# Kernel tuning notes

Measured on AMD Instinct MI355X. Metric: run time of the kernel, lower is better.

The kernel has to match this reference:

```python
import jax, jax.numpy as jnp
import numpy as np


def setup_inputs() -> dict:
    key = jax.random.key(0)
    ks = jax.random.split(key, 16)
    B, S, D = 2, 2048, 1024
    H, SH, RH = 16, 1, 3
    hd = D // H
    w = 1.0 / np.sqrt(D)
    return {
        "x": jax.random.normal(ks[0], (B, S, D), jnp.float32),
        "Wq": jax.random.normal(ks[1], (D, D), jnp.float32) * w,
        "bq": jnp.zeros((D,), jnp.float32),
        "Wk": jax.random.normal(ks[2], (D, D), jnp.float32) * w,
        "bk": jnp.zeros((D,), jnp.float32),
        "Wv": jax.random.normal(ks[3], (D, D), jnp.float32) * w,
        "bv": jnp.zeros((D,), jnp.float32),
        "Wproj": jax.random.normal(ks[4], (D, D), jnp.float32) * w,
        "bproj": jnp.zeros((D,), jnp.float32),
        "Wr": jax.random.normal(ks[5], (D, H - SH), jnp.float32) * w,
        "br": jnp.zeros((H - SH,), jnp.float32),
        "Ws": jax.random.normal(ks[6], (D, 2), jnp.float32) * w,
        "bs": jnp.zeros((2,), jnp.float32),
        "temperature": jnp.zeros((H, 1, 1), jnp.float32),
        "query_embedding": jax.random.truncated_normal(ks[7], -2.0, 2.0, (H, 1, hd), jnp.float32) * 0.02,
        "num_heads": H,
        "shared_heads": SH,
        "routed_heads": RH,
    }


def reference(x, Wq, bq, Wk, bk, Wv, bv, Wproj, bproj, Wr, br, Ws, bs,
              temperature, query_embedding, num_heads, shared_heads, routed_heads):
    B, S, D = x.shape
    H = num_heads
    hd = D // H

    def split_heads(t):  # [B,S,D] -> [B,H,S,hd]
        return t.reshape(B, S, H, hd).transpose(0, 2, 1, 3)

    q = split_heads(x @ Wq + bq)
    k = split_heads(x @ Wk + bk)
    v = split_heads(x @ Wv + bv)

    # L2-normalize q along head_dim, add learned query embedding, scale by softplus(temperature)
    q_norm = q * jax.lax.rsqrt(jnp.sum(q * q, axis=-1, keepdims=True) + 1e-12)
    q_scaled = (q_norm + query_embedding[None]) * jax.nn.softplus(temperature)[None]

    attn = jnp.einsum('bhqd,bhkd->bhqk', q_scaled, k) / jnp.sqrt(jnp.float32(hd))
    attn = jax.nn.softmax(attn, axis=-1)
    o = jnp.einsum('bhqk,bhkd->bhqd', attn, v)
    o = o.transpose(0, 2, 1, 3).reshape(B, S, D)  # [B,S,D]

    # Routed-head gating via top-k router
    gates = jax.nn.softmax(o @ Wr + br, axis=-1)          # [B,S,H-SH]
    _, idx = jax.lax.top_k(gates, routed_heads)           # [B,S,RH]
    mask = jax.nn.one_hot(idx, H - shared_heads, dtype=gates.dtype).sum(axis=2)
    routed_gates = gates * mask * jnp.float32(routed_heads)

    # Shared-head gating
    sw = jax.nn.softmax(o @ Ws + bs, axis=-1)             # [B,S,2]
    shared_gates = sw * jnp.float32(shared_heads)
    w0 = sw * 2.0
    shared_gates = w0[..., 0:1] * shared_gates
    routed_gates = w0[..., 1:2] * routed_gates
    masked_gates = jnp.concatenate([shared_gates, routed_gates], axis=-1)

    # einsum('bnh,bnd->bnd') sums over h: scales o by sum of gates
    o = masked_gates.sum(axis=-1, keepdims=True) * o
    return o @ Wproj + bproj
```

## Files before the change

### kernel.cpp

```cpp
#include <hip/hip_runtime.h>
#include <hip/hip_bf16.h>

typedef unsigned short ushort_t;
typedef unsigned int uint_t;

typedef __attribute__((ext_vector_type(8))) short bf8;
typedef __attribute__((ext_vector_type(4))) float f4;
typedef __attribute__((ext_vector_type(16))) float f16v;

__device__ __forceinline__ float bf2f(ushort_t u) {
    unsigned int x = ((unsigned int)u) << 16;
    return __uint_as_float(x);
}
__device__ __forceinline__ ushort_t f2bf(float f) {
    unsigned int x = __float_as_uint(f);
    unsigned int r = x + 0x7fffu + ((x >> 16) & 1u);
    return (ushort_t)(r >> 16);
}
__device__ __forceinline__ uint_t pack2bf(float a, float b) {
    return (uint_t)f2bf(a) | ((uint_t)f2bf(b) << 16);
}
__device__ __forceinline__ uint_t pack2bf_fast(float a, float b) {
    uint_t au = __float_as_uint(a) + 0x8000u;
    uint_t bu = __float_as_uint(b) + 0x8000u;
    return __builtin_amdgcn_perm(bu, au, 0x07060302);
}
__device__ __forceinline__ float exp2_fast(float x) {
    float r; asm("v_exp_f32 %0, %1" : "=v"(r) : "v"(x)); return r;
}
__device__ __forceinline__ uint_t cvtpk_bf16(float lo, float hi) {
    uint_t r; asm("v_cvt_pk_bf16_f32 %0, %1, %2" : "=v"(r) : "v"(lo), "v"(hi)); return r;
}
__device__ __forceinline__ void pl32swap(uint_t &a, uint_t &b) {
    asm("v_permlane32_swap_b32 %0, %1" : "+v"(a), "+v"(b));
}

__device__ __forceinline__ void gl2lds16(const ushort_t* g, ushort_t* l) {
    __builtin_amdgcn_global_load_lds(
        (const __attribute__((address_space(1))) void*)g,
        (__attribute__((address_space(3))) void*)l, 16, 0, 0);
}

__device__ __forceinline__ void waitl0() {
    asm volatile("s_waitcnt lgkmcnt(0)" ::: "memory");
    __builtin_amdgcn_sched_barrier(0);
}

__global__ __launch_bounds__(256)
void prep(const float* __restrict__ x, ushort_t* __restrict__ xb,
          const float* __restrict__ Wr, const float* __restrict__ Ws,
          ushort_t* __restrict__ Wg,
          const float* __restrict__ W0, const float* __restrict__ W1,
          const float* __restrict__ W2, const float* __restrict__ W3,
          ushort_t* __restrict__ T0, ushort_t* __restrict__ T1,
          ushort_t* __restrict__ T2, ushort_t* __restrict__ T3)
{
    __shared__ float tile[32][33];
    int bid = blockIdx.x;
    int t = threadIdx.x;
    if (bid < 4096) {
        int i = bid * 256 + t;
        float4 v = ((const float4*)x)[i];
        uint2 o;
        o.x = pack2bf(v.x, v.y);
        o.y = pack2bf(v.z, v.w);
        ((uint2*)xb)[i] = o;
    } else if (bid < 4224) {
        int idx = (bid - 4096) * 256 + t;
        int c = idx >> 10, d = idx & 1023;
        float v = 0.f;
        if (c < 15) v = Wr[(size_t)d * 15 + c];
        else if (c < 17) v = Ws[(size_t)d * 2 + (c - 15)];
        Wg[idx] = f2bf(v);
    } else {
        int idx = bid - 4224;
        int z = idx >> 10, r10 = idx & 1023;
        int k0 = (r10 & 31) * 32, n0 = (r10 >> 5) * 32;
        const float* W; ushort_t* T;
        switch (z) {
            case 0: W = W0; T = T0; break;
            case 1: W = W1; T = T1; break;
            case 2: W = W2; T = T2; break;
            default: W = W3; T = T3; break;
        }
        int r = t >> 3, c4 = (t & 7) * 4;
        float4 v = *(const float4*)&W[(size_t)(k0 + r) * 1024 + n0 + c4];
        tile[r][c4 + 0] = v.x; tile[r][c4 + 1] = v.y;
        tile[r][c4 + 2] = v.z; tile[r][c4 + 3] = v.w;
        __syncthreads();
        int n = t >> 3, kk = (t & 7) * 4;
        uint2 o;
        o.x = pack2bf(tile[kk][n], tile[kk + 1][n]);
        o.y = pack2bf(tile[kk + 2][n], tile[kk + 3][n]);
        *(uint2*)&T[(size_t)(n0 + n) * 1024 + k0 + kk] = o;
    }
}

__global__ __launch_bounds__(256)
void gemmQKV(const ushort_t* __restrict__ A, const ushort_t* __restrict__ Wt3,
             const float* __restrict__ bq, const float* __restrict__ bk,
             const float* __restrict__ bv,
             ushort_t* __restrict__ Qb, ushort_t* __restrict__ Kw,
             ushort_t* __restrict__ VTw,
             const float* __restrict__ temp, const float* __restrict__ emb)
{
    const int K = 1024;
    __shared__ ushort_t As[128 * 64];
    __shared__ ushort_t Bs[64 * 64];

    int t = threadIdx.x;
    int m0 = blockIdx.x * 128;
    int y = blockIdx.y;
    int region = y >> 4;
    int n0r = (y & 15) * 64;
    int head = y & 15;

    int lane = t & 63, w = t >> 6;
    int lm = lane & 15, quad = lane >> 4;
    int wm = w * 32;

    f4 acc[8] = {};

    int srow = t >> 3;
    int schunk = ((t & 7) ^ (srow & 7)) * 8;
    const ushort_t* pA = &A[(size_t)(m0 + srow) * K + schunk];
    const ushort_t* pB = &Wt3[(size_t)(y * 64 + srow) * K + schunk];
    const size_t rstep = (size_t)32 * K;

    for (int k0 = 0; k0 < K; k0 += 64) {
        #pragma unroll
        for (int j = 0; j < 4; j++)
            gl2lds16(pA + j * rstep, &As[(t + j * 256) * 8]);
        #pragma unroll
        for (int j = 0; j < 2; j++)
            gl2lds16(pB + j * rstep, &Bs[(t + j * 256) * 8]);
        pA += 64; pB += 64;
        __syncthreads();

        #pragma unroll
        for (int ks = 0; ks < 2; ks++) {
            int rc = ((ks * 4 + quad) ^ (lm & 7)) * 8;
            bf8 af[2], bfr[4];
            #pragma unroll
            for (int mi = 0; mi < 2; mi++)
                af[mi] = *(bf8*)&As[(wm + mi * 16 + lm) * 64 + rc];
            #pragma unroll
            for (int ni = 0; ni < 4; ni++)
                bfr[ni] = *(bf8*)&Bs[(ni * 16 + lm) * 64 + rc];
            if (region == 2) {
                #pragma unroll
                for (int mi = 0; mi < 2; mi++)
                #pragma unroll
                for (int ni = 0; ni < 4; ni++)
                    acc[mi * 4 + ni] = __builtin_amdgcn_mfma_f32_16x16x32_bf16(af[mi], bfr[ni], acc[mi * 4 + ni], 0, 0, 0);
            } else {
                #pragma unroll
                for (int ni = 0; ni < 4; ni++)
                #pragma unroll
                for (int mi = 0; mi < 2; mi++)
                    acc[ni * 2 + mi] = __builtin_amdgcn_mfma_f32_16x16x32_bf16(bfr[ni], af[mi], acc[ni * 2 + mi], 0, 0, 0);
            }
        }
        __syncthreads();
    }

    if (region == 0) {
        float sp = log1pf(__expf(temp[head]));
        float qs = sp * 0.18033688011112042f;
        f4 bv4[4], ev4[4];
        #pragma unroll
        for (int ni = 0; ni < 4; ni++) {
            bv4[ni] = *(const f4*)&bq[n0r + ni * 16 + quad * 4];
            ev4[ni] = *(const f4*)&emb[head * 64 + ni * 16 + quad * 4];
        }
        #pragma unroll
        for (int mi = 0; mi < 2; mi++) {
            float v[4][4];
            float ss = 0.f;
            #pragma unroll
            for (int ni = 0; ni < 4; ni++)
            #pragma unroll
            for (int i = 0; i < 4; i++) {
                v[ni][i] = acc[ni * 2 + mi][i] + bv4[ni][i];
                ss += v[ni][i] * v[ni][i];
            }
            ss += __shfl_xor(ss, 16, 64);
            ss += __shfl_xor(ss, 32, 64);
            float rs = rsqrtf(ss + 1e-12f);
            int tok = m0 + wm + mi * 16 + lm;
            int b = tok >> 11, s = tok & 2047;
            size_t rowb = (((size_t)(b * 16 + head)) * 2048 + s) * 64;
            #pragma unroll
            for (int ni = 0; ni < 4; ni++) {
                uint2 o;
                o.x = pack2bf((v[ni][0] * rs + ev4[ni][0]) * qs,
                              (v[ni][1] * rs + ev4[ni][1]) * qs);
                o.y = pack2bf((v[ni][2] * rs + ev4[ni][2]) * qs,
                              (v[ni][3] * rs + ev4[ni][3]) * qs);
                *(uint2*)&Qb[rowb + ni * 16 + quad * 4] = o;
            }
        }
    } else if (region == 1) {
        f4 bv4[4];
        #pragma unroll
        for (int ni = 0; ni < 4; ni++)
            bv4[ni] = *(const f4*)&bk[n0r + ni * 16 + quad * 4];
        #pragma unroll
        for (int mi = 0; mi < 2; mi++) {
            int tok = m0 + wm + mi * 16 + lm;
            int b = tok >> 11, s = tok & 2047;
            size_t rowb = (((size_t)(b * 16 + head)) * 2048 + s) * 64;
            #pragma unroll
            for (int ni = 0; ni < 4; ni++) {
                uint2 o;
                o.x = pack2bf(acc[ni * 2 + mi][0] + bv4[ni][0], acc[ni * 2 + mi][1] + bv4[ni][1]);
                o.y = pack2bf(acc[ni * 2 + mi][2] + bv4[ni][2], acc[ni * 2 + mi][3] + bv4[ni][3]);
                *(uint2*)&Kw[rowb + ni * 16 + quad * 4] = o;
            }
        }
    } else {
        float bvv[4];
        #pragma unroll
        for (int ni = 0; ni < 4; ni++) bvv[ni] = bv[n0r + ni * 16 + lm];
        #pragma unroll
        for (int mi = 0; mi < 2; mi++) {
            int gr0 = m0 + wm + mi * 16 + quad * 4;
            int b = gr0 >> 11, s0 = gr0 & 2047;
            #pragma unroll
            for (int ni = 0; ni < 4; ni++) {
                int d = ni * 16 + lm;
                uint2 o;
                o.x = pack2bf(acc[mi * 4 + ni][0] + bvv[ni], acc[mi * 4 + ni][1] + bvv[ni]);
                o.y = pack2bf(acc[mi * 4 + ni][2] + bvv[ni], acc[mi * 4 + ni][3] + bvv[ni]);
                *(uint2*)&VTw[(((size_t)(b * 16 + head)) * 64 + d) * 2048 + s0] = o;
            }
        }
    }
}

__global__ __launch_bounds__(256)
void gemmP(const ushort_t* __restrict__ A, const ushort_t* __restrict__ Wt,
           const float* __restrict__ bias, const float* __restrict__ G,
           float* __restrict__ out, int M, int N, int K)
{
    __shared__ ushort_t As[64 * 64];
    __shared__ ushort_t Bs[128 * 64];

    int t = threadIdx.x;
    int m0 = blockIdx.x * 64, n0 = blockIdx.y * 128;
    int lane = t & 63, w = t >> 6;
    int lm = lane & 15, quad = lane >> 4;
    int wm = (w >> 1) * 32, wn = (w & 1) * 64;

    f4 acc[4][2] = {};

    int srow = t >> 3;
    int schunk = ((t & 7) ^ (srow & 7)) * 8;
    const ushort_t* pA = &A[(size_t)(m0 + srow) * K + schunk];
    const ushort_t* pB = &Wt[(size_t)(n0 + srow) * K + schunk];
    const size_t rstep = (size_t)32 * K;

    for (int k0 = 0; k0 < K; k0 += 64) {
        gl2lds16(pA, &As[t * 8]);
        gl2lds16(pA + rstep, &As[(t + 256) * 8]);
        #pragma unroll
        for (int j = 0; j < 4; j++)
            gl2lds16(pB + j * rstep, &Bs[(t + j * 256) * 8]);
        pA += 64; pB += 64;
        __syncthreads();

        #pragma unroll
        for (int ks = 0; ks < 2; ks++) {
            int rc = ((ks * 4 + quad) ^ (lm & 7)) * 8;
            bf8 af[2], bfr[4];
            #pragma unroll
            for (int mi = 0; mi < 2; mi++)
                af[mi] = *(bf8*)&As[(wm + mi * 16 + lm) * 64 + rc];
            #pragma unroll
            for (int ni = 0; ni < 4; ni++)
                bfr[ni] = *(bf8*)&Bs[(wn + ni * 16 + lm) * 64 + rc];
            #pragma unroll
            for (int ni = 0; ni < 4; ni++)
            #pragma unroll
            for (int mi = 0; mi < 2; mi++)
                acc[ni][mi] = __builtin_amdgcn_mfma_f32_16x16x32_bf16(bfr[ni], af[mi], acc[ni][mi], 0, 0, 0);
        }
        __syncthreads();
    }

    f4 bv4[4];
    #pragma unroll
    for (int ni = 0; ni < 4; ni++)
        bv4[ni] = *(const f4*)&bias[n0 + wn + ni * 16 + quad * 4];
    #pragma unroll
    for (int mi = 0; mi < 2; mi++) {
        int tok = m0 + wm + mi * 16 + lm;
        float g = G[tok];
        size_t rowb = (size_t)tok * N + n0 + wn;
        #pragma unroll
        for (int ni = 0; ni < 4; ni++) {
            f4 o;
            #pragma unroll
            for (int i = 0; i < 4; i++) o[i] = g * acc[ni][mi][i] + bv4[ni][i];
            *(f4*)&out[rowb + ni * 16 + quad * 4] = o;
        }
    }
}

__global__ __launch_bounds__(256)
void attn(const ushort_t* __restrict__ Q, const ushort_t* __restrict__ K,
          const ushort_t* __restrict__ VT, ushort_t* __restrict__ Opart,
          float* __restrict__ Lw, int kps)
{
    __shared__ ushort_t Ks[2][64 * 72];
    __shared__ ushort_t Vt[2][64 * 72];

    int t = threadIdx.x, lane = t & 63, w = t >> 6;
    int l31 = lane & 31;
    uint_t hi = lane >> 5;
    int bid = blockIdx.x;
    int bh = bid & 31, qt = (bid >> 5) & 15, ks = bid >> 9;
    size_t base = (size_t)bh * 2048 * 64;

    int tok = qt * 128 + w * 32 + l31;
    const ushort_t* qp = &Q[base + (size_t)tok * 64 + hi * 8];
    bf8 qa[4];
    #pragma unroll
    for (int c = 0; c < 4; c++) qa[c] = *(const bf8*)(qp + c * 16);

    float l_part = 0.f;
    f16v o_acc[2] = {};

    int sr = t >> 3, sc = (t & 7) * 8;
    const ushort_t* kp = &K[base + (size_t)(ks * kps + sr) * 64 + sc];
    const ushort_t* vp = &VT[base + (size_t)sr * 2048 + ks * kps + sc];

    uint4 rk0 = *(const uint4*)(kp);
    uint4 rk1 = *(const uint4*)(kp + 32 * 64);
    uint4 rv0 = *(const uint4*)(vp);
    uint4 rv1 = *(const uint4*)(vp + 32 * 2048);
    kp += 64 * 64; vp += 64;
    *(uint4*)&Ks[0][sr * 72 + sc] = rk0;
    *(uint4*)&Ks[0][(sr + 32) * 72 + sc] = rk1;
    *(uint4*)&Vt[0][sr * 72 + sc] = rv0;
    *(uint4*)&Vt[0][(sr + 32) * 72 + sc] = rv1;
    rk0 = *(const uint4*)(kp);
    rk1 = *(const uint4*)(kp + 32 * 64);
    rv0 = *(const uint4*)(vp);
    rv1 = *(const uint4*)(vp + 32 * 2048);
    kp += 64 * 64; vp += 64;
    __syncthreads();

    int cur = 0;
    int iters = kps >> 6;
    for (int it = 0; it < iters; ++it) {
        {
            ushort_t* Kw_ = &Ks[cur ^ 1][0];
            ushort_t* Vw_ = &Vt[cur ^ 1][0];
            *(uint4*)&Kw_[sr * 72 + sc] = rk0;
            *(uint4*)&Kw_[(sr + 32) * 72 + sc] = rk1;
            *(uint4*)&Vw_[sr * 72 + sc] = rv0;
            *(uint4*)&Vw_[(sr + 32) * 72 + sc] = rv1;
        }
        rk0 = *(const uint4*)(kp);
        rk1 = *(const uint4*)(kp + 32 * 64);
        rv0 = *(const uint4*)(vp);
        rv1 = *(const uint4*)(vp + 32 * 2048);
        kp += 64 * 64; vp += 64;

        const ushort_t* Kr = &Ks[cur][0];
        const ushort_t* Vr = &Vt[cur][0];

        bf8 pf[4];
        #pragma unroll
        for (int kt2 = 0; kt2 < 2; kt2++) {
            f16v s = {};
            #pragma unroll
            for (int c = 0; c < 4; c++) {
                bf8 kf = *(bf8*)&Kr[(kt2 * 32 + l31) * 72 + c * 16 + hi * 8];
                s = __builtin_amdgcn_mfma_f32_32x32x16_bf16(kf, qa[c], s, 0, 0, 0);
            }
            uint_t px[4], py[4];
            #pragma unroll
            for (int g = 0; g < 4; g++) {
                float p0 = exp2_fast(s[g * 4 + 0]);
                float p1 = exp2_fast(s[g * 4 + 1]);
                float p2 = exp2_fast(s[g * 4 + 2]);
                float p3 = exp2_fast(s[g * 4 + 3]);
                l_part += (p0 + p1) + (p2 + p3);
                px[g] = cvtpk_bf16(p0, p1);
                py[g] = cvtpk_bf16(p2, p3);
            }
            #pragma unroll
            for (int cc = 0; cc < 2; cc++) {
                uint_t ax = px[2 * cc], bx = px[2 * cc + 1];
                uint_t ay = py[2 * cc], by = py[2 * cc + 1];
                pl32swap(ax, bx);
                pl32swap(ay, by);
                uint4 u;
                u.x = ax; u.y = ay; u.z = bx; u.w = by;
                pf[kt2 * 2 + cc] = *(bf8*)&u;
            }
        }

        #pragma unroll
        for (int c = 0; c < 4; c++) {
            #pragma unroll
            for (int dt = 0; dt < 2; dt++) {
                bf8 vf = *(bf8*)&Vr[(dt * 32 + l31) * 72 + c * 16 + hi * 8];
                o_acc[dt] = __builtin_amdgcn_mfma_f32_32x32x16_bf16(vf, pf[c], o_acc[dt], 0, 0, 0);
            }
        }
        __syncthreads();
        cur ^= 1;
    }

    l_part += __shfl_xor(l_part, 32, 64);
    if (hi == 0) Lw[((size_t)ks * 32 + bh) * 2048 + tok] = l_part;

    size_t pbase = (((size_t)(ks * 32 + bh)) * 2048 + tok) * 64;
    #pragma unroll
    for (int dt = 0; dt < 2; dt++)
    #pragma unroll
    for (int g = 0; g < 4; g++) {
        int d0 = dt * 32 + g * 8 + hi * 4;
        uint2 o;
        o.x = pack2bf_fast(o_acc[dt][g * 4 + 0], o_acc[dt][g * 4 + 1]);
        o.y = pack2bf_fast(o_acc[dt][g * 4 + 2], o_acc[dt][g * 4 + 3]);
        *(uint2*)&Opart[pbase + d0] = o;
    }
}

__global__ __launch_bounds__(256)
void fuseCR(const ushort_t* __restrict__ Opart, const float* __restrict__ Lw,
            const ushort_t* __restrict__ Wg, const float* __restrict__ br,
            const float* __restrict__ bs, ushort_t* __restrict__ Ob,
            float* __restrict__ G, int splits)
{
    __shared__ ushort_t Obs[16 * 1032];
    __shared__ float rl_s[16][16];
    __shared__ float Ls[16][21];

    int t = threadIdx.x;
    int tokg0 = blockIdx.x * 16;
    int b = tokg0 >> 11, st0 = tokg0 & 2047;

    {
        int h = t >> 4, tt = t & 15;
        size_t row = (size_t)(b * 16 + h) * 2048 + st0 + tt;
        float l = 0.f;
        #pragma unroll 4
        for (int s = 0; s < splits; s++) l += Lw[(size_t)s * 65536 + row];
        rl_s[h][tt] = 1.f / l;
    }
    __syncthreads();

    {
        int tt = t >> 4, dc = (t & 15) * 4;
        #pragma unroll 4
        for (int h = 0; h < 16; h++) {
            size_t rbase = ((size_t)(b * 16 + h) * 2048 + st0 + tt) * 64 + dc;
            float v0 = 0.f, v1 = 0.f, v2 = 0.f, v3 = 0.f;
            #pragma unroll 4
            for (int s = 0; s < splits; s++) {
                uint2 p = *(const uint2*)&Opart[(size_t)s * 4194304 + rbase];
                v0 += bf2f(p.x & 0xffff);
                v1 += bf2f(p.x >> 16);
                v2 += bf2f(p.y & 0xffff);
                v3 += bf2f(p.y >> 16);
            }
            float rl = rl_s[h][tt];
            v0 *= rl; v1 *= rl; v2 *= rl; v3 *= rl;
            uint2 o;
            o.x = pack2bf(v0, v1);
            o.y = pack2bf(v2, v3);
            *(uint2*)&Obs[tt * 1032 + h * 64 + dc] = o;
            *(uint2*)&Ob[((size_t)(tokg0 + tt)) * 1024 + h * 64 + dc] = o;
        }
    }
    __syncthreads();

    if (t < 64) {
        int lm = t & 15, quad = t >> 4;
        const ushort_t* b0p = &Wg[(size_t)lm * 1024 + quad * 8];
        const ushort_t* b1p = &Wg[(size_t)(16 + lm) * 1024 + quad * 8];
        f4 acc0 = {}, acc1 = {};
        for (int k0 = 0; k0 < 1024; k0 += 32) {
            bf8 a  = *(const bf8*)&Obs[lm * 1032 + k0 + quad * 8];
            bf8 b0 = *(const bf8*)(b0p + k0);
            bf8 b1 = *(const bf8*)(b1p + k0);
            acc0 = __builtin_amdgcn_mfma_f32_16x16x32_bf16(a, b0, acc0, 0, 0, 0);
            acc1 = __builtin_amdgcn_mfma_f32_16x16x32_bf16(a, b1, acc1, 0, 0, 0);
        }
        #pragma unroll
        for (int i = 0; i < 4; i++) {
            int tl = quad * 4 + i;
            Ls[tl][lm] = acc0[i];
            if (lm == 0) Ls[tl][16] = acc1[i];
        }
        waitl0();

        if (t < 16) {
            float v[15];
            float mx = -1e30f;
            #pragma unroll
            for (int c = 0; c < 15; c++) { v[c] = Ls[t][c] + br[c]; mx = fmaxf(mx, v[c]); }
            float sum = 0.f;
            #pragma unroll
            for (int c = 0; c < 15; c++) { v[c] = __expf(v[c] - mx); sum += v[c]; }
            float inv = 1.f / sum;
            float t3 = 0.f;
            for (int r = 0; r < 3; r++) {
                int bi = 0; float bv = -1e30f;
                #pragma unroll
                for (int c = 0; c < 15; c++) if (v[c] > bv) { bv = v[c]; bi = c; }
                t3 += bv; v[bi] = -1e30f;
            }
            t3 *= inv;
            float a0 = Ls[t][15] + bs[0], a1 = Ls[t][16] + bs[1];
            float m2 = fmaxf(a0, a1);
            float e0 = __expf(a0 - m2), e1 = __expf(a1 - m2);
            G[tokg0 + t] = (2.f * e0 + 6.f * e1 * t3) / (e0 + e1);
        }
    }
}

extern "C" void kernel_launch(void* const* d_in, const int* in_sizes, int n_in,
                              void* d_out, int out_size, void* d_ws, size_t ws_size,
                              hipStream_t stream)
{
    const float* x     = (const float*)d_in[0];
    const float* Wq    = (const float*)d_in[1];
    const float* bq    = (const float*)d_in[2];
    const float* Wk    = (const float*)d_in[3];
    const float* bk    = (const float*)d_in[4];
    const float* Wv    = (const float*)d_in[5];
    const float* bv    = (const float*)d_in[6];
    const float* Wproj = (const float*)d_in[7];
    const float* bproj = (const float*)d_in[8];
    const float* Wr    = (const float*)d_in[9];
    const float* br    = (const float*)d_in[10];
    const float* Ws    = (const float*)d_in[11];
    const float* bs    = (const float*)d_in[12];
    const float* temp  = (const float*)d_in[13];
    const float* emb   = (const float*)d_in[14];

    const int M = 4096, N = 1024, Kd = 1024;

    char* ws = (char*)d_ws;
    ushort_t* Kw    = (ushort_t*)ws;
    ushort_t* VTw   = (ushort_t*)(ws + 8388608);
    ushort_t* Qb    = (ushort_t*)(ws + 16777216);
    ushort_t* Wtp   = (ushort_t*)(ws + 25165824);
    float*    Gw    = (float*)(ws + 27262976);
    ushort_t* Wg    = (ushort_t*)(ws + 27279360);
    float*    Lw    = (float*)(ws + 27344896);
    ushort_t* Wt3   = (ushort_t*)(ws + 27869184);
    ushort_t* Opart = (ushort_t*)(ws + 27869184);
    ushort_t* xb    = (ushort_t*)(ws + 34160640);
    ushort_t* Ob    = Qb;

    const int SK = 2;

    prep<<<8320, 256, 0, stream>>>(x, xb, Wr, Ws, Wg, Wq, Wk, Wv, Wproj,
        Wt3, Wt3 + 1048576, Wt3 + 2097152, Wtp);

    gemmQKV<<<dim3(32, 48), 256, 0, stream>>>(xb, Wt3, bq, bk, bv,
        Qb, Kw, VTw, temp, emb);

    attn<<<512 * SK, 256, 0, stream>>>(Qb, Kw, VTw, Opart, Lw, 2048 / SK);

    fuseCR<<<256, 256, 0, stream>>>(Opart, Lw, Wg, br, bs, Ob, Gw, SK);

    gemmP<<<dim3(64, 8), 256, 0, stream>>>(Ob, Wtp, bproj, Gw, (float*)d_out, M, N, Kd);
}
```

Baseline: 235.1 us.

## Stage attention K/V tiles via direct global-to-LDS loads with XOR swizzle

Replaces the register-staged K/V double-buffer in the attention kernel with direct global-to-LDS 16-byte loads (gl2lds16). The padded 72-wide LDS rows become an unpadded 64-wide layout with an XOR column swizzle to avoid bank conflicts. The aim is to save VGPRs and drop the separate LDS store instructions while keeping the prefetch overlap. The risk is that correct ordering now depends on async LDS-load completion before the barrier, and the swizzle math has to match how gl2lds16 places data per lane.

```diff
diff --git a/kernel.cpp b/kernel.cpp
--- a/kernel.cpp
+++ b/kernel.cpp
@@ -312,12 +312,13 @@
           const ushort_t* __restrict__ VT, ushort_t* __restrict__ Opart,
           float* __restrict__ Lw, int kps)
 {
-    __shared__ ushort_t Ks[2][64 * 72];
-    __shared__ ushort_t Vt[2][64 * 72];
+    __shared__ ushort_t Ks[2][64 * 64];
+    __shared__ ushort_t Vt[2][64 * 64];
 
     int t = threadIdx.x, lane = t & 63, w = t >> 6;
     int l31 = lane & 31;
     uint_t hi = lane >> 5;
+    int x7 = l31 & 7;
     int bid = blockIdx.x;
     int bh = bid & 31, qt = (bid >> 5) & 15, ks = bid >> 9;
     size_t base = (size_t)bh * 2048 * 64;
@@ -331,42 +332,31 @@
     float l_part = 0.f;
     f16v o_acc[2] = {};
 
-    int sr = t >> 3, sc = (t & 7) * 8;
-    const ushort_t* kp = &K[base + (size_t)(ks * kps + sr) * 64 + sc];
-    const ushort_t* vp = &VT[base + (size_t)sr * 2048 + ks * kps + sc];
-
-    uint4 rk0 = *(const uint4*)(kp);
-    uint4 rk1 = *(const uint4*)(kp + 32 * 64);
-    uint4 rv0 = *(const uint4*)(vp);
-    uint4 rv1 = *(const uint4*)(vp + 32 * 2048);
-    kp += 64 * 64; vp += 64;
-    *(uint4*)&Ks[0][sr * 72 + sc] = rk0;
-    *(uint4*)&Ks[0][(sr + 32) * 72 + sc] = rk1;
-    *(uint4*)&Vt[0][sr * 72 + sc] = rv0;
-    *(uint4*)&Vt[0][(sr + 32) * 72 + sc] = rv1;
-    rk0 = *(const uint4*)(kp);
-    rk1 = *(const uint4*)(kp + 32 * 64);
-    rv0 = *(const uint4*)(vp);
-    rv1 = *(const uint4*)(vp + 32 * 2048);
+    int sr = t >> 3;
+    int sch = ((t & 7) ^ (sr & 7)) * 8;
+    const ushort_t* kp = &K[base + (size_t)(ks * kps + sr) * 64 + sch];
+    const ushort_t* vp = &VT[base + (size_t)sr * 2048 + ks * kps + sch];
+    const size_t kR = (size_t)32 * 64;
+    const size_t vR = (size_t)32 * 2048;
+
+    gl2lds16(kp,      &Ks[0][t * 8]);
+    gl2lds16(kp + kR, &Ks[0][(t + 256) * 8]);
+    gl2lds16(vp,      &Vt[0][t * 8]);
+    gl2lds16(vp + vR, &Vt[0][(t + 256) * 8]);
     kp += 64 * 64; vp += 64;
     __syncthreads();
 
     int cur = 0;
     int iters = kps >> 6;
     for (int it = 0; it < iters; ++it) {
-        {
-            ushort_t* Kw_ = &Ks[cur ^ 1][0];
-            ushort_t* Vw_ = &Vt[cur ^ 1][0];
-            *(uint4*)&Kw_[sr * 72 + sc] = rk0;
-            *(uint4*)&Kw_[(sr + 32) * 72 + sc] = rk1;
-            *(uint4*)&Vw_[sr * 72 + sc] = rv0;
-            *(uint4*)&Vw_[(sr + 32) * 72 + sc] = rv1;
-        }
-        rk0 = *(const uint4*)(kp);
-        rk1 = *(const uint4*)(kp + 32 * 64);
-        rv0 = *(const uint4*)(vp);
-        rv1 = *(const uint4*)(vp + 32 * 2048);
-        kp += 64 * 64; vp += 64;
+        if (it + 1 < iters) {
+            int nb = cur ^ 1;
+            gl2lds16(kp,      &Ks[nb][t * 8]);
+            gl2lds16(kp + kR, &Ks[nb][(t + 256) * 8]);
+            gl2lds16(vp,      &Vt[nb][t * 8]);
+            gl2lds16(vp + vR, &Vt[nb][(t + 256) * 8]);
+            kp += 64 * 64; vp += 64;
+        }
 
         const ushort_t* Kr = &Ks[cur][0];
         const ushort_t* Vr = &Vt[cur][0];
@@ -377,7 +367,8 @@
             f16v s = {};
             #pragma unroll
             for (int c = 0; c < 4; c++) {
-                bf8 kf = *(bf8*)&Kr[(kt2 * 32 + l31) * 72 + c * 16 + hi * 8];
+                int sw = ((c * 2 + (int)hi) ^ x7) * 8;
+                bf8 kf = *(bf8*)&Kr[(kt2 * 32 + l31) * 64 + sw];
                 s = __builtin_amdgcn_mfma_f32_32x32x16_bf16(kf, qa[c], s, 0, 0, 0);
             }
             uint_t px[4], py[4];
@@ -407,7 +398,8 @@
         for (int c = 0; c < 4; c++) {
             #pragma unroll
             for (int dt = 0; dt < 2; dt++) {
-                bf8 vf = *(bf8*)&Vr[(dt * 32 + l31) * 72 + c * 16 + hi * 8];
+                int sw = ((c * 2 + (int)hi) ^ x7) * 8;
+                bf8 vf = *(bf8*)&Vr[(dt * 32 + l31) * 64 + sw];
                 o_acc[dt] = __builtin_amdgcn_mfma_f32_32x32x16_bf16(vf, pf[c], o_acc[dt], 0, 0, 0);
             }
         }
```

New measurement: 238.4 us. No clear change (+1.4%).
